# Optimization experiments

Measured on AMD Instinct MI355X. Metric: run time of the kernel, lower is better.

Reference implementation:

```python
import jax, jax.numpy as jnp
import numpy as np

B, N, FA, FP, C = 64, 64, 75, 14, 128


def _mlp2(x, W0, b0, W1, b1):
    # two lazy-Linear + ReLU sub-layers (n_sub_layer=2)
    h = jax.nn.relu(x @ W0 + b0)
    return jax.nn.relu(h @ W1 + b1)


def setup_inputs() -> dict:
    key = jax.random.key(0)
    ks = jax.random.split(key, 32)
    w = lambda k, s: jax.random.normal(k, s, jnp.float32) * 0.05
    inp = {
        "atom_x": jax.random.normal(ks[0], (B, N, FA), jnp.float32),
        "pair_x": jax.random.normal(ks[1], (B, N * N, FP), jnp.float32),
        # atom_to_atom: FA -> C -> C
        "a2a_W0": w(ks[2], (FA, C)), "a2a_b0": w(ks[3], (C,)),
        "a2a_W1": w(ks[4], (C, C)), "a2a_b1": w(ks[5], (C,)),
        # pair_to_atom: FP -> C -> C
        "p2a_W0": w(ks[6], (FP, C)), "p2a_b0": w(ks[7], (C,)),
        "p2a_W1": w(ks[8], (C, C)), "p2a_b1": w(ks[9], (C,)),
        # atom_layer: 2C -> C -> C
        "al_W0": w(ks[10], (2 * C, C)), "al_b0": w(ks[11], (C,)),
        "al_W1": w(ks[12], (C, C)), "al_b1": w(ks[13], (C,)),
        # atom_to_pair (weights shared across both orderings): 2FA -> C -> C
        "a2p_W0": w(ks[14], (2 * FA, C)), "a2p_b0": w(ks[15], (C,)),
        "a2p_W1": w(ks[16], (C, C)), "a2p_b1": w(ks[17], (C,)),
        # pair_to_pair: FP -> C -> C
        "p2p_W0": w(ks[18], (FP, C)), "p2p_b0": w(ks[19], (C,)),
        "p2p_W1": w(ks[20], (C, C)), "p2p_b1": w(ks[21], (C,)),
        # pair_layer: 2C -> C -> C
        "pl_W0": w(ks[22], (2 * C, C)), "pl_b0": w(ks[23], (C,)),
        "pl_W1": w(ks[24], (C, C)), "pl_b1": w(ks[25], (C,)),
    }
    return inp


def reference(atom_x, pair_x,
              a2a_W0, a2a_b0, a2a_W1, a2a_b1,
              p2a_W0, p2a_b0, p2a_W1, p2a_b1,
              al_W0, al_b0, al_W1, al_b1,
              a2p_W0, a2p_b0, a2p_W1, a2p_b1,
              p2p_W0, p2p_b0, p2p_W1, p2p_b1,
              pl_W0, pl_b0, pl_W1, pl_b1):
    b, n, fa = atom_x.shape
    # --- atom branch ---
    a0 = _mlp2(atom_x, a2a_W0, a2a_b0, a2a_W1, a2a_b1)            # [B,N,C]
    a1 = _mlp2(pair_x, p2a_W0, p2a_b0, p2a_W1, p2a_b1)            # [B,N*N,C]
    a1 = a1.reshape(b, n, n, -1).sum(axis=2)                      # PairToAtom sum
    a = jnp.concatenate([a0, a1], axis=-1)                        # [B,N,2C]
    next_atom = jax.nn.relu(_mlp2(a, al_W0, al_b0, al_W1, al_b1))  # extra relu per forward
    # --- pair branch ---
    rep = jnp.broadcast_to(atom_x[:, None, :, :], (b, n, n, fa))  # atom_repeat
    til = jnp.broadcast_to(atom_x[:, :, None, :], (b, n, n, fa))  # atom_tile
    pr0 = jnp.concatenate([til, rep], axis=-1).reshape(b, n * n, 2 * fa)
    pr1 = jnp.concatenate([rep, til], axis=-1).reshape(b, n * n, 2 * fa)
    p0 = (_mlp2(pr0, a2p_W0, a2p_b0, a2p_W1, a2p_b1)
          + _mlp2(pr1, a2p_W0, a2p_b0, a2p_W1, a2p_b1))            # [B,N*N,C]
    p1 = _mlp2(pair_x, p2p_W0, p2p_b0, p2p_W1, p2p_b1)            # [B,N*N,C]
    p = jnp.concatenate([p0, p1], axis=-1)                        # [B,N*N,2C]
    next_pair = jax.nn.relu(_mlp2(p, pl_W0, pl_b0, pl_W1, pl_b1))
    return (next_atom, next_pair)
```

## Files before the change

### kernel.cpp

```cpp
#include <hip/hip_runtime.h>
#include <hip/hip_bf16.h>

typedef unsigned short u16;
typedef unsigned int u32;
typedef __attribute__((ext_vector_type(8))) __bf16 bf16x8;
typedef __attribute__((ext_vector_type(4))) float f32x4;

#define B_ 64
#define N_ 64
#define FA_ 75
#define FP_ 14
#define C_ 128

__device__ float g_A0[4096 * 128];
__device__ float g_A1[4096 * 128];
__device__ float g_TB[4096 * 256];
__device__ u16   g_Wf[208896];

#define OFF_AA0   0
#define OFF_AA1   12288
#define OFF_APT   28672
#define OFF_APB   40960
#define OFF_PA0   53248
#define OFF_PA1   57344
#define OFF_AL0   73728
#define OFF_AL1   106496
#define OFF_AP1   122880
#define OFF_PP0   139264
#define OFF_PP1   143360
#define OFF_PL0T  159744
#define OFF_PL0B  176128
#define OFF_PL1   192512

__device__ __forceinline__ float bf2f(u16 a) {
    union { u32 u; float f; } v; v.u = ((u32)a) << 16; return v.f;
}
__device__ __forceinline__ u16 f2bf(float f) {
    union { float f; u32 u; } v; v.f = f;
    u32 r = v.u + 0x7fffu + ((v.u >> 16) & 1u);
    return (u16)(r >> 16);
}
#if __has_builtin(__builtin_amdgcn_cvt_pk_bf16_f32)
__device__ __forceinline__ u32 f2bf_pk(float a, float b) {
    auto r = __builtin_amdgcn_cvt_pk_bf16_f32(a, b);
    if constexpr (sizeof(r) == 4) {
        union { decltype(r) v; u32 u; } c; c.v = r; return c.u;
    } else {
        return (u32)f2bf(a) | ((u32)f2bf(b) << 16);
    }
}
#else
__device__ __forceinline__ u32 f2bf_pk(float a, float b) {
    return (u32)f2bf(a) | ((u32)f2bf(b) << 16);
}
#endif

__device__ __forceinline__ bool detect_isbf(const void* __restrict__ atom) {
    u32 wrd = ((const u32*)atom)[threadIdx.x & 63];
    u32 ex = (wrd >> 7) & 0xffu;
    unsigned long long m = __ballot(ex >= 113u && ex <= 133u);
    return __popcll(m) >= 32;
}

__device__ __forceinline__ float ldf(const void* p, size_t i, bool isbf) {
    if (isbf) return bf2f(((const u16*)p)[i]);
    return ((const float*)p)[i];
}
__device__ __forceinline__ f32x4 ldf4(const void* p, int i, bool isbf) {
    f32x4 r;
    if (isbf) {
        const u16* q = (const u16*)p + i;
        r[0] = bf2f(q[0]); r[1] = bf2f(q[1]); r[2] = bf2f(q[2]); r[3] = bf2f(q[3]);
    } else {
        r = *(const f32x4*)((const float*)p + i);
    }
    return r;
}
__device__ __forceinline__ uint4 pack8(const void* p, size_t base, int kmax, int k0, bool isbf) {
    uint4 u;
    if (isbf) {
        const u16* q = (const u16*)p + base;
        u16 h[8];
#pragma unroll
        for (int j = 0; j < 8; ++j) h[j] = (k0 + j < kmax) ? q[k0 + j] : (u16)0;
        u.x = (u32)h[0] | ((u32)h[1] << 16); u.y = (u32)h[2] | ((u32)h[3] << 16);
        u.z = (u32)h[4] | ((u32)h[5] << 16); u.w = (u32)h[6] | ((u32)h[7] << 16);
    } else {
        const float* q = (const float*)p + base;
        float f[8];
#pragma unroll
        for (int j = 0; j < 8; ++j) f[j] = (k0 + j < kmax) ? q[k0 + j] : 0.f;
        u.x = f2bf_pk(f[0], f[1]); u.y = f2bf_pk(f[2], f[3]);
        u.z = f2bf_pk(f[4], f[5]); u.w = f2bf_pk(f[6], f[7]);
    }
    return u;
}

__global__ __launch_bounds__(256) void prep_w(
    const void* atom,
    const void* aaW0, const void* aaW1, const void* apW0,
    const void* paW0, const void* paW1, const void* alW0, const void* alW1,
    const void* apW1, const void* ppW0, const void* ppW1,
    const void* plW0, const void* plW1) {
    const bool isbf = detect_isbf(atom);
    const void* srcs[14] = {aaW0, aaW1, apW0, apW0, paW0, paW1, alW0, alW1,
                            apW1, ppW0, ppW1, plW0, plW0, plW1};
    const int Ktab[14]  = {75, 128, 75, 75, 14, 128, 256, 128, 128, 14, 128, 128, 128, 128};
    const int KStab[14] = {3, 4, 3, 3, 1, 4, 8, 4, 4, 1, 4, 4, 4, 4};
    const int rofft[14] = {0, 0, 0, 75, 0, 0, 0, 0, 0, 0, 0, 0, 128, 0};
    const int baset[14] = {OFF_AA0, OFF_AA1, OFF_APT, OFF_APB, OFF_PA0, OFF_PA1,
                           OFF_AL0, OFF_AL1, OFF_AP1, OFF_PP0, OFF_PP1,
                           OFF_PL0T, OFF_PL0B, OFF_PL1};
    int gid = blockIdx.x * 256 + threadIdx.x;
    int j = 0, s = gid;
    while (j < 14 && s >= KStab[j] * 512) { s -= KStab[j] * 512; ++j; }
    if (j >= 14) return;
    int lane = s & 63, rest = s >> 6;
    int ks = rest % KStab[j], mt = rest / KStab[j];
    int m = mt * 16 + (lane & 15), q = lane >> 4;
    float f[8];
#pragma unroll
    for (int jj = 0; jj < 8; ++jj) {
        int k = ks * 32 + q * 8 + jj;
        f[jj] = (k < Ktab[j]) ? ldf(srcs[j], (size_t)(rofft[j] + k) * 128 + m, isbf) : 0.f;
    }
    uint4 u;
    u.x = f2bf_pk(f[0], f[1]); u.y = f2bf_pk(f[2], f[3]);
    u.z = f2bf_pk(f[4], f[5]); u.w = f2bf_pk(f[6], f[7]);
    *(uint4*)&g_Wf[(size_t)baset[j] + (size_t)s * 8] = u;
}

__device__ __forceinline__ bf16x8 as_bf(uint4 u) {
    union { uint4 u; bf16x8 b; } cv; cv.u = u; return cv.b;
}
template<int KS, int NT>
__device__ __forceinline__ void gemm2(const u16* __restrict__ wf,
                                      const u16* __restrict__ bF,
                                      int mt0, int lane, f32x4 (&acc)[2][NT]) {
#pragma unroll
    for (int ks = 0; ks < KS; ++ks) {
        bf16x8 a0 = *(const bf16x8*)(wf + (((mt0    ) * KS + ks) * 64 + lane) * 8);
        bf16x8 a1 = *(const bf16x8*)(wf + (((mt0 + 1) * KS + ks) * 64 + lane) * 8);
#pragma unroll
        for (int nt = 0; nt < NT; ++nt) {
            bf16x8 b = *(const bf16x8*)(bF + ((nt * KS + ks) * 64 + lane) * 8);
            acc[0][nt] = __builtin_amdgcn_mfma_f32_16x16x32_bf16(a0, b, acc[0][nt], 0, 0, 0);
            acc[1][nt] = __builtin_amdgcn_mfma_f32_16x16x32_bf16(a1, b, acc[1][nt], 0, 0, 0);
        }
    }
}
template<int KS>
__device__ __forceinline__ void loadA2(const u16* __restrict__ wf, int mt0, int lane,
                                       uint4 (&aw)[2][KS]) {
#pragma unroll
    for (int ks = 0; ks < KS; ++ks) {
        aw[0][ks] = *(const uint4*)(wf + (((mt0    ) * KS + ks) * 64 + lane) * 8);
        aw[1][ks] = *(const uint4*)(wf + (((mt0 + 1) * KS + ks) * 64 + lane) * 8);
    }
}
template<int KS, int NT>
__device__ __forceinline__ void gemm2r(const uint4 (&aw)[2][KS],
                                       const u16* __restrict__ bF,
                                       int lane, f32x4 (&acc)[2][NT]) {
#pragma unroll
    for (int ks = 0; ks < KS; ++ks) {
        bf16x8 a0 = as_bf(aw[0][ks]);
        bf16x8 a1 = as_bf(aw[1][ks]);
#pragma unroll
        for (int nt = 0; nt < NT; ++nt) {
            bf16x8 b = *(const bf16x8*)(bF + ((nt * KS + ks) * 64 + lane) * 8);
            acc[0][nt] = __builtin_amdgcn_mfma_f32_16x16x32_bf16(a0, b, acc[0][nt], 0, 0, 0);
            acc[1][nt] = __builtin_amdgcn_mfma_f32_16x16x32_bf16(a1, b, acc[1][nt], 0, 0, 0);
        }
    }
}

__device__ __forceinline__ void barrier_lgkm() {
    asm volatile("s_waitcnt lgkmcnt(0)" ::: "memory");
    __builtin_amdgcn_s_barrier();
    asm volatile("" ::: "memory");
}

__device__ __forceinline__ void frag_store(u16* dstF, int KSd, int nt, int mt, int lane, f32x4 v) {
    int c = lane & 15, quad = lane >> 4;
    int lp = c + 16 * ((2 * mt + (quad >> 1)) & 3);
    int ks = mt >> 1;
    uint2 u; u.x = f2bf_pk(v[0], v[1]); u.y = f2bf_pk(v[2], v[3]);
    *(uint2*)(dstF + (((nt * KSd + ks) * 64 + lp) * 8 + (quad & 1) * 4)) = u;
}

__device__ __forceinline__ void store_out4(void* outp, size_t elem, f32x4 v, bool isbf) {
    if (isbf) {
        uint2 u; u.x = f2bf_pk(v[0], v[1]); u.y = f2bf_pk(v[2], v[3]);
        *(uint2*)((u16*)outp + elem) = u;
    } else {
        *(f32x4*)((float*)outp + elem) = v;
    }
}

#define EPI_RELU_STORE(ACC, BB0, BB1, DST, NTN) do {                             \
    _Pragma("unroll") for (int ii = 0; ii < 2; ++ii) {                           \
        f32x4 bb_ = ii ? (BB1) : (BB0);                                          \
        _Pragma("unroll") for (int nt_ = 0; nt_ < NTN; ++nt_) {                  \
            f32x4 v_;                                                            \
            _Pragma("unroll") for (int r_ = 0; r_ < 4; ++r_) {                   \
                float x_ = ACC[ii][nt_][r_] + bb_[r_];                           \
                v_[r_] = x_ > 0.f ? x_ : 0.f;                                    \
            }                                                                    \
            frag_store(DST, 4, nt_, mt0 + ii, lane, v_);                         \
        }                                                                        \
    }                                                                            \
} while (0)

__global__ __launch_bounds__(256) void atom_pre(
    const void* __restrict__ atom,
    const void* __restrict__ aaB0, const void* __restrict__ aaB1) {
    __shared__ __align__(16) u16 sXF[2 * 3 * 64 * 8];
    __shared__ __align__(16) u16 sHF[2 * 4 * 64 * 8];
    const bool isbf = detect_isbf(atom);
    const int t = threadIdx.x, lane = t & 63, w = t >> 6;
    const int quad = lane >> 4;
    const int r0g = blockIdx.x * 32;
    for (int s = t; s < 2 * 3 * 64; s += 256) {
        int lane_s = s & 63, rest = s >> 6;
        int ks = rest % 3, nt = rest / 3;
        int n = nt * 16 + (lane_s & 15), q = lane_s >> 4;
        *(uint4*)&sXF[s * 8] = pack8(atom, (size_t)(r0g + n) * FA_, FA_, ks * 32 + q * 8, isbf);
    }
    __syncthreads();
    const int mt0 = 2 * w;
    {
        f32x4 bb0 = ldf4(aaB0, mt0 * 16 + quad * 4, isbf);
        f32x4 bb1 = ldf4(aaB0, (mt0 + 1) * 16 + quad * 4, isbf);
        f32x4 acc[2][2];
#pragma unroll
        for (int ii = 0; ii < 2; ++ii)
#pragma unroll
            for (int nt = 0; nt < 2; ++nt) acc[ii][nt] = (f32x4){0.f, 0.f, 0.f, 0.f};
        gemm2<3, 2>(g_Wf + OFF_AA0, sXF, mt0, lane, acc);
        EPI_RELU_STORE(acc, bb0, bb1, sHF, 2);
    }
    __syncthreads();
    {
        f32x4 bb0 = ldf4(aaB1, mt0 * 16 + quad * 4, isbf);
        f32x4 bb1 = ldf4(aaB1, (mt0 + 1) * 16 + quad * 4, isbf);
        f32x4 acc[2][2];
#pragma unroll
        for (int ii = 0; ii < 2; ++ii)
#pragma unroll
            for (int nt = 0; nt < 2; ++nt) acc[ii][nt] = (f32x4){0.f, 0.f, 0.f, 0.f};
        gemm2<4, 2>(g_Wf + OFF_AA1, sHF, mt0, lane, acc);
        int c = lane & 15;
#pragma unroll
        for (int ii = 0; ii < 2; ++ii) {
            int mt = mt0 + ii;
            f32x4 bb = ii ? bb1 : bb0;
#pragma unroll
            for (int nt = 0; nt < 2; ++nt) {
                f32x4 v;
#pragma unroll
                for (int r = 0; r < 4; ++r) { float x = acc[ii][nt][r] + bb[r]; v[r] = x > 0.f ? x : 0.f; }
                *(f32x4*)&g_A0[(size_t)(r0g + nt * 16 + c) * 128 + mt * 16 + quad * 4] = v;
            }
        }
    }
    {
        f32x4 accT[2][2], accB[2][2];
#pragma unroll
        for (int ii = 0; ii < 2; ++ii)
#pragma unroll
            for (int nt = 0; nt < 2; ++nt) { accT[ii][nt] = (f32x4){0.f,0.f,0.f,0.f}; accB[ii][nt] = (f32x4){0.f,0.f,0.f,0.f}; }
        gemm2<3, 2>(g_Wf + OFF_APT, sXF, mt0, lane, accT);
        gemm2<3, 2>(g_Wf + OFF_APB, sXF, mt0, lane, accB);
        int c = lane & 15;
#pragma unroll
        for (int ii = 0; ii < 2; ++ii) {
            int mt = mt0 + ii;
#pragma unroll
            for (int nt = 0; nt < 2; ++nt) {
                size_t row = (size_t)(r0g + nt * 16 + c);
                *(f32x4*)&g_TB[row * 256 + mt * 16 + quad * 4] = accT[ii][nt];
                *(f32x4*)&g_TB[row * 256 + 128 + mt * 16 + quad * 4] = accB[ii][nt];
            }
        }
    }
}

__global__ __launch_bounds__(256) void atom_layer(
    const void* __restrict__ atom,
    const void* __restrict__ alB0, const void* __restrict__ alB1,
    void* __restrict__ out) {
    __shared__ __align__(16) u16 sXF[1 * 8 * 64 * 8];
    __shared__ __align__(16) u16 sHF[1 * 4 * 64 * 8];
    const bool isbf = detect_isbf(atom);
    const int t = threadIdx.x, lane = t & 63, w = t >> 6;
    const int quad = lane >> 4;
    const int r0g = blockIdx.x * 16;
    for (int s = t; s < 8 * 64; s += 256) {
        int lane_s = s & 63, ks = s >> 6;
        int n = lane_s & 15, q = lane_s >> 4;
        int k0 = ks * 32 + q * 8;
        const float* src = (k0 < 128) ? &g_A0[(size_t)(r0g + n) * 128 + k0]
                                      : &g_A1[(size_t)(r0g + n) * 128 + (k0 - 128)];
        f32x4 f0 = *(const f32x4*)src, f1 = *(const f32x4*)(src + 4);
        uint4 u;
        u.x = f2bf_pk(f0[0], f0[1]); u.y = f2bf_pk(f0[2], f0[3]);
        u.z = f2bf_pk(f1[0], f1[1]); u.w = f2bf_pk(f1[2], f1[3]);
        *(uint4*)&sXF[s * 8] = u;
    }
    __syncthreads();
    const int mt0 = 2 * w;
    {
        f32x4 bb0 = ldf4(alB0, mt0 * 16 + quad * 4, isbf);
        f32x4 bb1 = ldf4(alB0, (mt0 + 1) * 16 + quad * 4, isbf);
        f32x4 acc[2][1];
#pragma unroll
        for (int ii = 0; ii < 2; ++ii) acc[ii][0] = (f32x4){0.f, 0.f, 0.f, 0.f};
        gemm2<8, 1>(g_Wf + OFF_AL0, sXF, mt0, lane, acc);
        EPI_RELU_STORE(acc, bb0, bb1, sHF, 1);
    }
    __syncthreads();
    {
        f32x4 bb0 = ldf4(alB1, mt0 * 16 + quad * 4, isbf);
        f32x4 bb1 = ldf4(alB1, (mt0 + 1) * 16 + quad * 4, isbf);
        f32x4 acc[2][1];
#pragma unroll
        for (int ii = 0; ii < 2; ++ii) acc[ii][0] = (f32x4){0.f, 0.f, 0.f, 0.f};
        gemm2<4, 1>(g_Wf + OFF_AL1, sHF, mt0, lane, acc);
        int c = lane & 15;
#pragma unroll
        for (int ii = 0; ii < 2; ++ii) {
            int mt = mt0 + ii;
            f32x4 bb = ii ? bb1 : bb0;
            f32x4 v;
#pragma unroll
            for (int r = 0; r < 4; ++r) { float x = acc[ii][0][r] + bb[r]; v[r] = x > 0.f ? x : 0.f; }
            store_out4(out, (size_t)(r0g + c) * 128 + mt * 16 + quad * 4, v, isbf);
        }
    }
}

__global__ __launch_bounds__(256, 3) void pair_fused(
    const void* __restrict__ atom,
    const void* __restrict__ pairx,
    const void* __restrict__ apB0, const void* __restrict__ apB1,
    const void* __restrict__ ppB0, const void* __restrict__ ppB1,
    const void* __restrict__ plB0, const void* __restrict__ plB1,
    const void* __restrict__ paB0, const void* __restrict__ paB1,
    void* __restrict__ out) {
    __shared__ __align__(16) u16 sX1[4 * 4 * 64 * 8];
    __shared__ __align__(16) u16 sX2[4 * 4 * 64 * 8];
    __shared__ __align__(16) u16 sR [4 * 4 * 64 * 8];
    __shared__ __align__(16) u16 sPr[4 * 1 * 64 * 8];
    const bool isbf = detect_isbf(atom);
    const int t = threadIdx.x, lane = t & 63, w = t >> 6;
    const int quad = lane >> 4, c = lane & 15;
    const int bx = blockIdx.x;
    const int b = bx >> 6, i = bx & 63;
    const int trow = b * 64;
    const size_t prow0 = (size_t)b * 4096 + (size_t)i * 64;
    const int mt0 = 2 * w;

    {
        int lane_s = t & 63, nt = t >> 6;
        int n = nt * 16 + (lane_s & 15), q = lane_s >> 4;
        *(uint4*)&sPr[t * 8] = pack8(pairx, (prow0 + n) * FP_, FP_, q * 8, isbf);
    }
    {
        const int ksg = t >> 6;
        const int k0 = ksg * 32 + quad * 8;
        const int rc = c;
        const float* TBi = &g_TB[(size_t)(trow + i) * 256 + k0];
        f32x4 t0 = *(const f32x4*)TBi,        t1 = *(const f32x4*)(TBi + 4);
        f32x4 o0 = *(const f32x4*)(TBi + 128), o1 = *(const f32x4*)(TBi + 132);
        f32x4 b0a = ldf4(apB0, k0, isbf), b0b = ldf4(apB0, k0 + 4, isbf);
        float Tip[8], Bip[8];
#pragma unroll
        for (int r = 0; r < 4; ++r) {
            Tip[r] = t0[r] + b0a[r]; Tip[4 + r] = t1[r] + b0b[r];
            Bip[r] = o0[r] + b0a[r]; Bip[4 + r] = o1[r] + b0b[r];
        }
#pragma unroll
        for (int nt = 0; nt < 4; ++nt) {
            int n = nt * 16 + rc;
            const float* Bj = &g_TB[(size_t)(trow + n) * 256 + k0];
            f32x4 j0 = *(const f32x4*)Bj,        j1 = *(const f32x4*)(Bj + 4);
            f32x4 j2 = *(const f32x4*)(Bj + 128), j3 = *(const f32x4*)(Bj + 132);
            float v0[8], v1[8];
#pragma unroll
            for (int r = 0; r < 4; ++r) {
                float x0 = Tip[r] + j2[r];      v0[r]     = x0 > 0.f ? x0 : 0.f;
                float x1 = Tip[4 + r] + j3[r];  v0[4 + r] = x1 > 0.f ? x1 : 0.f;
                float y0 = j0[r] + Bip[r];      v1[r]     = y0 > 0.f ? y0 : 0.f;
                float y1 = j1[r] + Bip[4 + r];  v1[4 + r] = y1 > 0.f ? y1 : 0.f;
            }
            uint4 u0, u1;
            u0.x = f2bf_pk(v0[0], v0[1]); u0.y = f2bf_pk(v0[2], v0[3]);
            u0.z = f2bf_pk(v0[4], v0[5]); u0.w = f2bf_pk(v0[6], v0[7]);
            u1.x = f2bf_pk(v1[0], v1[1]); u1.y = f2bf_pk(v1[2], v1[3]);
            u1.z = f2bf_pk(v1[4], v1[5]); u1.w = f2bf_pk(v1[6], v1[7]);
            int slot = ((nt * 4 + ksg) * 64 + lane) * 8;
            *(uint4*)&sX1[slot] = u0;
            *(uint4*)&sX2[slot] = u1;
        }
    }
    uint4 aAP1[2][4]; loadA2<4>(g_Wf + OFF_AP1, mt0, lane, aAP1);
    barrier_lgkm();
    {
        f32x4 bb0 = ldf4(apB1, mt0 * 16 + quad * 4, isbf);
        f32x4 bb1 = ldf4(apB1, (mt0 + 1) * 16 + quad * 4, isbf);
        f32x4 aA[2][4], aB[2][4];
#pragma unroll
        for (int ii = 0; ii < 2; ++ii)
#pragma unroll
            for (int nt = 0; nt < 4; ++nt) { aA[ii][nt] = (f32x4){0.f,0.f,0.f,0.f}; aB[ii][nt] = (f32x4){0.f,0.f,0.f,0.f}; }
        gemm2r<4, 4>(aAP1, sX1, lane, aA);
        gemm2r<4, 4>(aAP1, sX2, lane, aB);
#pragma unroll
        for (int ii = 0; ii < 2; ++ii) {
            int mt = mt0 + ii;
            f32x4 bb = ii ? bb1 : bb0;
#pragma unroll
            for (int nt = 0; nt < 4; ++nt) {
                f32x4 v;
#pragma unroll
                for (int r = 0; r < 4; ++r) {
                    float x = aA[ii][nt][r] + bb[r];
                    float y = aB[ii][nt][r] + bb[r];
                    v[r] = (x > 0.f ? x : 0.f) + (y > 0.f ? y : 0.f);
                }
                frag_store(sR, 4, nt, mt, lane, v);
            }
        }
    }
    f32x4 aH[2][4], aPA[2][4];
    {
        uint4 aPP0[2][1]; loadA2<1>(g_Wf + OFF_PP0, mt0, lane, aPP0);
        uint4 aPA0[2][1]; loadA2<1>(g_Wf + OFF_PA0, mt0, lane, aPA0);
#pragma unroll
        for (int ii = 0; ii < 2; ++ii)
#pragma unroll
            for (int nt = 0; nt < 4; ++nt) { aH[ii][nt] = (f32x4){0.f,0.f,0.f,0.f}; aPA[ii][nt] = (f32x4){0.f,0.f,0.f,0.f}; }
        gemm2r<1, 4>(aPP0, sPr, lane, aH);
        gemm2r<1, 4>(aPA0, sPr, lane, aPA);
    }
    uint4 aPL0T[2][4]; loadA2<4>(g_Wf + OFF_PL0T, mt0, lane, aPL0T);
    barrier_lgkm();
    f32x4 C3[2][4];
#pragma unroll
    for (int ii = 0; ii < 2; ++ii)
#pragma unroll
        for (int nt = 0; nt < 4; ++nt) C3[ii][nt] = (f32x4){0.f, 0.f, 0.f, 0.f};
    gemm2r<4, 4>(aPL0T, sR, lane, C3);
    {
        f32x4 bb0 = ldf4(ppB0, mt0 * 16 + quad * 4, isbf);
        f32x4 bb1 = ldf4(ppB0, (mt0 + 1) * 16 + quad * 4, isbf);
        EPI_RELU_STORE(aH, bb0, bb1, sX1, 4);
    }
    {
        f32x4 bb0 = ldf4(paB0, mt0 * 16 + quad * 4, isbf);
        f32x4 bb1 = ldf4(paB0, (mt0 + 1) * 16 + quad * 4, isbf);
        EPI_RELU_STORE(aPA, bb0, bb1, sX2, 4);
    }
    uint4 aPP1[2][4]; loadA2<4>(g_Wf + OFF_PP1, mt0, lane, aPP1);
    uint4 aPA1[2][4]; loadA2<4>(g_Wf + OFF_PA1, mt0, lane, aPA1);
    barrier_lgkm();
    {
        f32x4 aP[2][4], aA1[2][4];
#pragma unroll
        for (int ii = 0; ii < 2; ++ii)
#pragma unroll
            for (int nt = 0; nt < 4; ++nt) { aP[ii][nt] = (f32x4){0.f,0.f,0.f,0.f}; aA1[ii][nt] = (f32x4){0.f,0.f,0.f,0.f}; }
        gemm2r<4, 4>(aPP1, sX1, lane, aP);
        gemm2r<4, 4>(aPA1, sX2, lane, aA1);
        {
            f32x4 pb0 = ldf4(paB1, mt0 * 16 + quad * 4, isbf);
            f32x4 pb1 = ldf4(paB1, (mt0 + 1) * 16 + quad * 4, isbf);
#pragma unroll
            for (int ii = 0; ii < 2; ++ii) {
                int mt = mt0 + ii;
                f32x4 bb = ii ? pb1 : pb0;
                f32x4 ssum = (f32x4){0.f, 0.f, 0.f, 0.f};
#pragma unroll
                for (int nt = 0; nt < 4; ++nt)
#pragma unroll
                    for (int r = 0; r < 4; ++r) {
                        float x = aA1[ii][nt][r] + bb[r];
                        ssum[r] += (x > 0.f ? x : 0.f);
                    }
#pragma unroll
                for (int m = 1; m < 16; m <<= 1)
#pragma unroll
                    for (int r = 0; r < 4; ++r) ssum[r] += __shfl_xor(ssum[r], m, 64);
                if ((lane & 15) == 0)
                    *(f32x4*)&g_A1[(size_t)bx * 128 + mt * 16 + quad * 4] = ssum;
            }
        }
        f32x4 bb0 = ldf4(ppB1, mt0 * 16 + quad * 4, isbf);
        f32x4 bb1 = ldf4(ppB1, (mt0 + 1) * 16 + quad * 4, isbf);
        EPI_RELU_STORE(aP, bb0, bb1, sR, 4);
    }
    uint4 aPL0B[2][4]; loadA2<4>(g_Wf + OFF_PL0B, mt0, lane, aPL0B);
    barrier_lgkm();
    gemm2r<4, 4>(aPL0B, sR, lane, C3);
    {
        f32x4 bb0 = ldf4(plB0, mt0 * 16 + quad * 4, isbf);
        f32x4 bb1 = ldf4(plB0, (mt0 + 1) * 16 + quad * 4, isbf);
        EPI_RELU_STORE(C3, bb0, bb1, sX1, 4);
    }
    uint4 aPL1[2][4]; loadA2<4>(g_Wf + OFF_PL1, mt0, lane, aPL1);
    barrier_lgkm();
    {
        f32x4 bb0 = ldf4(plB1, mt0 * 16 + quad * 4, isbf);
        f32x4 bb1 = ldf4(plB1, (mt0 + 1) * 16 + quad * 4, isbf);
        f32x4 aO[2][4];
#pragma unroll
        for (int ii = 0; ii < 2; ++ii)
#pragma unroll
            for (int nt = 0; nt < 4; ++nt) aO[ii][nt] = (f32x4){0.f, 0.f, 0.f, 0.f};
        gemm2r<4, 4>(aPL1, sX1, lane, aO);
        const size_t NA = (size_t)B_ * N_ * C_;
#pragma unroll
        for (int ii = 0; ii < 2; ++ii) {
            int mt = mt0 + ii;
            f32x4 bb = ii ? bb1 : bb0;
#pragma unroll
            for (int nt = 0; nt < 4; ++nt) {
                f32x4 v;
#pragma unroll
                for (int r = 0; r < 4; ++r) { float x = aO[ii][nt][r] + bb[r]; v[r] = x > 0.f ? x : 0.f; }
                store_out4(out, NA + (prow0 + nt * 16 + c) * 128 + mt * 16 + quad * 4, v, isbf);
            }
        }
    }
}

extern "C" void kernel_launch(void* const* d_in, const int* in_sizes, int n_in,
                              void* d_out, int out_size, void* d_ws, size_t ws_size,
                              hipStream_t stream) {
    const void* atom  = d_in[0];
    const void* pairx = d_in[1];
    const void* aaW0 = d_in[2];  const void* aaB0 = d_in[3];
    const void* aaW1 = d_in[4];  const void* aaB1 = d_in[5];
    const void* paW0 = d_in[6];  const void* paB0 = d_in[7];
    const void* paW1 = d_in[8];  const void* paB1 = d_in[9];
    const void* alW0 = d_in[10]; const void* alB0 = d_in[11];
    const void* alW1 = d_in[12]; const void* alB1 = d_in[13];
    const void* apW0 = d_in[14]; const void* apB0 = d_in[15];
    const void* apW1 = d_in[16]; const void* apB1 = d_in[17];
    const void* ppW0 = d_in[18]; const void* ppB0 = d_in[19];
    const void* ppW1 = d_in[20]; const void* ppB1 = d_in[21];
    const void* plW0 = d_in[22]; const void* plB0 = d_in[23];
    const void* plW1 = d_in[24]; const void* plB1 = d_in[25];
    (void)d_ws; (void)ws_size; (void)in_sizes; (void)n_in; (void)out_size;

    prep_w<<<102, 256, 0, stream>>>(atom, aaW0, aaW1, apW0, paW0, paW1, alW0, alW1,
                                    apW1, ppW0, ppW1, plW0, plW1);
    atom_pre<<<128, 256, 0, stream>>>(atom, aaB0, aaB1);
    pair_fused<<<4096, 256, 0, stream>>>(atom, pairx, apB0, apB1, ppB0, ppB1,
                                         plB0, plB1, paB0, paB1, d_out);
    atom_layer<<<256, 256, 0, stream>>>(atom, alB0, alB1, d_out);
}
```

Before: 288.9 us.

## Fuse weight prep into atom pre-pass and raise wave priority around MFMA loops

Merges the weight-conversion kernel and the atom pre-pass into one launch. The first 76 blocks convert the weights the later kernels need, and the remaining blocks compute the atom branch, reading the FA-side weights directly from the raw inputs and converting them on the fly. This removes one kernel launch and its serialization point, at the cost of redundant per-block weight loads and conversion in the atom pre-pass. It also adds s_setprio around the MFMA GEMM calls in pair_fused to favour waves that are in their matrix phases.

```diff
diff --git a/kernel.cpp b/kernel.cpp
--- a/kernel.cpp
+++ b/kernel.cpp
@@ -17,10 +17,6 @@
 __device__ float g_TB[4096 * 256];
 __device__ u16   g_Wf[208896];
 
-#define OFF_AA0   0
-#define OFF_AA1   12288
-#define OFF_APT   28672
-#define OFF_APB   40960
 #define OFF_PA0   53248
 #define OFF_PA1   57344
 #define OFF_AL0   73728
@@ -95,39 +91,18 @@
     }
     return u;
 }
-
-__global__ __launch_bounds__(256) void prep_w(
-    const void* atom,
-    const void* aaW0, const void* aaW1, const void* apW0,
-    const void* paW0, const void* paW1, const void* alW0, const void* alW1,
-    const void* apW1, const void* ppW0, const void* ppW1,
-    const void* plW0, const void* plW1) {
-    const bool isbf = detect_isbf(atom);
-    const void* srcs[14] = {aaW0, aaW1, apW0, apW0, paW0, paW1, alW0, alW1,
-                            apW1, ppW0, ppW1, plW0, plW0, plW1};
-    const int Ktab[14]  = {75, 128, 75, 75, 14, 128, 256, 128, 128, 14, 128, 128, 128, 128};
-    const int KStab[14] = {3, 4, 3, 3, 1, 4, 8, 4, 4, 1, 4, 4, 4, 4};
-    const int rofft[14] = {0, 0, 0, 75, 0, 0, 0, 0, 0, 0, 0, 0, 128, 0};
-    const int baset[14] = {OFF_AA0, OFF_AA1, OFF_APT, OFF_APB, OFF_PA0, OFF_PA1,
-                           OFF_AL0, OFF_AL1, OFF_AP1, OFF_PP0, OFF_PP1,
-                           OFF_PL0T, OFF_PL0B, OFF_PL1};
-    int gid = blockIdx.x * 256 + threadIdx.x;
-    int j = 0, s = gid;
-    while (j < 14 && s >= KStab[j] * 512) { s -= KStab[j] * 512; ++j; }
-    if (j >= 14) return;
-    int lane = s & 63, rest = s >> 6;
-    int ks = rest % KStab[j], mt = rest / KStab[j];
-    int m = mt * 16 + (lane & 15), q = lane >> 4;
+__device__ __forceinline__ uint4 packW8(const void* W, int kmax, int rofft,
+                                        int k0, int m, bool isbf) {
     float f[8];
 #pragma unroll
-    for (int jj = 0; jj < 8; ++jj) {
-        int k = ks * 32 + q * 8 + jj;
-        f[jj] = (k < Ktab[j]) ? ldf(srcs[j], (size_t)(rofft[j] + k) * 128 + m, isbf) : 0.f;
+    for (int j = 0; j < 8; ++j) {
+        int k = k0 + j;
+        f[j] = (k < kmax) ? ldf(W, (size_t)(rofft + k) * 128 + m, isbf) : 0.f;
     }
     uint4 u;
     u.x = f2bf_pk(f[0], f[1]); u.y = f2bf_pk(f[2], f[3]);
     u.z = f2bf_pk(f[4], f[5]); u.w = f2bf_pk(f[6], f[7]);
-    *(uint4*)&g_Wf[(size_t)baset[j] + (size_t)s * 8] = u;
+    return u;
 }
 
 __device__ __forceinline__ bf16x8 as_bf(uint4 u) {
@@ -141,6 +116,24 @@
     for (int ks = 0; ks < KS; ++ks) {
         bf16x8 a0 = *(const bf16x8*)(wf + (((mt0    ) * KS + ks) * 64 + lane) * 8);
         bf16x8 a1 = *(const bf16x8*)(wf + (((mt0 + 1) * KS + ks) * 64 + lane) * 8);
+#pragma unroll
+        for (int nt = 0; nt < NT; ++nt) {
+            bf16x8 b = *(const bf16x8*)(bF + ((nt * KS + ks) * 64 + lane) * 8);
+            acc[0][nt] = __builtin_amdgcn_mfma_f32_16x16x32_bf16(a0, b, acc[0][nt], 0, 0, 0);
+            acc[1][nt] = __builtin_amdgcn_mfma_f32_16x16x32_bf16(a1, b, acc[1][nt], 0, 0, 0);
+        }
+    }
+}
+template<int KS, int NT>
+__device__ __forceinline__ void gemm2w(const void* W, int kmax, int rofft, bool isbf,
+                                       const u16* __restrict__ bF,
+                                       int mt0, int lane, f32x4 (&acc)[2][NT]) {
+    const int c = lane & 15, q = lane >> 4;
+#pragma unroll
+    for (int ks = 0; ks < KS; ++ks) {
+        int k0 = ks * 32 + q * 8;
+        bf16x8 a0 = as_bf(packW8(W, kmax, rofft, k0, mt0 * 16 + c, isbf));
+        bf16x8 a1 = as_bf(packW8(W, kmax, rofft, k0, (mt0 + 1) * 16 + c, isbf));
 #pragma unroll
         for (int nt = 0; nt < NT; ++nt) {
             bf16x8 b = *(const bf16x8*)(bF + ((nt * KS + ks) * 64 + lane) * 8);
@@ -212,15 +205,46 @@
     }                                                                            \
 } while (0)
 
-__global__ __launch_bounds__(256) void atom_pre(
-    const void* __restrict__ atom,
-    const void* __restrict__ aaB0, const void* __restrict__ aaB1) {
+__global__ __launch_bounds__(256) void pre_fused(
+    const void* atom,
+    const void* aaW0, const void* aaW1, const void* apW0,
+    const void* paW0, const void* paW1, const void* alW0, const void* alW1,
+    const void* apW1, const void* ppW0, const void* ppW1,
+    const void* plW0, const void* plW1,
+    const void* aaB0, const void* aaB1) {
     __shared__ __align__(16) u16 sXF[2 * 3 * 64 * 8];
     __shared__ __align__(16) u16 sHF[2 * 4 * 64 * 8];
     const bool isbf = detect_isbf(atom);
     const int t = threadIdx.x, lane = t & 63, w = t >> 6;
     const int quad = lane >> 4;
-    const int r0g = blockIdx.x * 32;
+    if (blockIdx.x < 76) {
+        const void* srcs[10] = {paW0, paW1, alW0, alW1, apW1, ppW0, ppW1,
+                                plW0, plW0, plW1};
+        const int Ktab[10]  = {14, 128, 256, 128, 128, 14, 128, 128, 128, 128};
+        const int KStab[10] = {1, 4, 8, 4, 4, 1, 4, 4, 4, 4};
+        const int rofft[10] = {0, 0, 0, 0, 0, 0, 0, 0, 128, 0};
+        const int baset[10] = {OFF_PA0, OFF_PA1, OFF_AL0, OFF_AL1, OFF_AP1,
+                               OFF_PP0, OFF_PP1, OFF_PL0T, OFF_PL0B, OFF_PL1};
+        int gid = blockIdx.x * 256 + t;
+        int j = 0, s = gid;
+        while (j < 10 && s >= KStab[j] * 512) { s -= KStab[j] * 512; ++j; }
+        if (j >= 10) return;
+        int ln = s & 63, rest = s >> 6;
+        int ks = rest % KStab[j], mt = rest / KStab[j];
+        int m = mt * 16 + (ln & 15), q = ln >> 4;
+        float f[8];
+#pragma unroll
+        for (int jj = 0; jj < 8; ++jj) {
+            int k = ks * 32 + q * 8 + jj;
+            f[jj] = (k < Ktab[j]) ? ldf(srcs[j], (size_t)(rofft[j] + k) * 128 + m, isbf) : 0.f;
+        }
+        uint4 u;
+        u.x = f2bf_pk(f[0], f[1]); u.y = f2bf_pk(f[2], f[3]);
+        u.z = f2bf_pk(f[4], f[5]); u.w = f2bf_pk(f[6], f[7]);
+        *(uint4*)&g_Wf[(size_t)baset[j] + (size_t)s * 8] = u;
+        return;
+    }
+    const int r0g = (blockIdx.x - 76) * 32;
     for (int s = t; s < 2 * 3 * 64; s += 256) {
         int lane_s = s & 63, rest = s >> 6;
         int ks = rest % 3, nt = rest / 3;
@@ -237,7 +261,7 @@
         for (int ii = 0; ii < 2; ++ii)
 #pragma unroll
             for (int nt = 0; nt < 2; ++nt) acc[ii][nt] = (f32x4){0.f, 0.f, 0.f, 0.f};
-        gemm2<3, 2>(g_Wf + OFF_AA0, sXF, mt0, lane, acc);
+        gemm2w<3, 2>(aaW0, 75, 0, isbf, sXF, mt0, lane, acc);
         EPI_RELU_STORE(acc, bb0, bb1, sHF, 2);
     }
     __syncthreads();
@@ -249,7 +273,7 @@
         for (int ii = 0; ii < 2; ++ii)
 #pragma unroll
             for (int nt = 0; nt < 2; ++nt) acc[ii][nt] = (f32x4){0.f, 0.f, 0.f, 0.f};
-        gemm2<4, 2>(g_Wf + OFF_AA1, sHF, mt0, lane, acc);
+        gemm2w<4, 2>(aaW1, 128, 0, isbf, sHF, mt0, lane, acc);
         int c = lane & 15;
 #pragma unroll
         for (int ii = 0; ii < 2; ++ii) {
@@ -270,8 +294,8 @@
         for (int ii = 0; ii < 2; ++ii)
 #pragma unroll
             for (int nt = 0; nt < 2; ++nt) { accT[ii][nt] = (f32x4){0.f,0.f,0.f,0.f}; accB[ii][nt] = (f32x4){0.f,0.f,0.f,0.f}; }
-        gemm2<3, 2>(g_Wf + OFF_APT, sXF, mt0, lane, accT);
-        gemm2<3, 2>(g_Wf + OFF_APB, sXF, mt0, lane, accB);
+        gemm2w<3, 2>(apW0, 75, 0, isbf, sXF, mt0, lane, accT);
+        gemm2w<3, 2>(apW0, 75, 75, isbf, sXF, mt0, lane, accB);
         int c = lane & 15;
 #pragma unroll
         for (int ii = 0; ii < 2; ++ii) {
@@ -414,8 +438,10 @@
         for (int ii = 0; ii < 2; ++ii)
 #pragma unroll
             for (int nt = 0; nt < 4; ++nt) { aA[ii][nt] = (f32x4){0.f,0.f,0.f,0.f}; aB[ii][nt] = (f32x4){0.f,0.f,0.f,0.f}; }
+        __builtin_amdgcn_s_setprio(1);
         gemm2r<4, 4>(aAP1, sX1, lane, aA);
         gemm2r<4, 4>(aAP1, sX2, lane, aB);
+        __builtin_amdgcn_s_setprio(0);
 #pragma unroll
         for (int ii = 0; ii < 2; ++ii) {
             int mt = mt0 + ii;
@@ -451,7 +477,9 @@
     for (int ii = 0; ii < 2; ++ii)
 #pragma unroll
         for (int nt = 0; nt < 4; ++nt) C3[ii][nt] = (f32x4){0.f, 0.f, 0.f, 0.f};
+    __builtin_amdgcn_s_setprio(1);
     gemm2r<4, 4>(aPL0T, sR, lane, C3);
+    __builtin_amdgcn_s_setprio(0);
     {
         f32x4 bb0 = ldf4(ppB0, mt0 * 16 + quad * 4, isbf);
         f32x4 bb1 = ldf4(ppB0, (mt0 + 1) * 16 + quad * 4, isbf);
@@ -471,8 +499,10 @@
         for (int ii = 0; ii < 2; ++ii)
 #pragma unroll
             for (int nt = 0; nt < 4; ++nt) { aP[ii][nt] = (f32x4){0.f,0.f,0.f,0.f}; aA1[ii][nt] = (f32x4){0.f,0.f,0.f,0.f}; }
+        __builtin_amdgcn_s_setprio(1);
         gemm2r<4, 4>(aPP1, sX1, lane, aP);
         gemm2r<4, 4>(aPA1, sX2, lane, aA1);
+        __builtin_amdgcn_s_setprio(0);
         {
             f32x4 pb0 = ldf4(paB1, mt0 * 16 + quad * 4, isbf);
             f32x4 pb1 = ldf4(paB1, (mt0 + 1) * 16 + quad * 4, isbf);
@@ -502,7 +532,9 @@
     }
     uint4 aPL0B[2][4]; loadA2<4>(g_Wf + OFF_PL0B, mt0, lane, aPL0B);
     barrier_lgkm();
+    __builtin_amdgcn_s_setprio(1);
     gemm2r<4, 4>(aPL0B, sR, lane, C3);
+    __builtin_amdgcn_s_setprio(0);
     {
         f32x4 bb0 = ldf4(plB0, mt0 * 16 + quad * 4, isbf);
         f32x4 bb1 = ldf4(plB0, (mt0 + 1) * 16 + quad * 4, isbf);
@@ -518,7 +550,9 @@
         for (int ii = 0; ii < 2; ++ii)
 #pragma unroll
             for (int nt = 0; nt < 4; ++nt) aO[ii][nt] = (f32x4){0.f, 0.f, 0.f, 0.f};
+        __builtin_amdgcn_s_setprio(1);
         gemm2r<4, 4>(aPL1, sX1, lane, aO);
+        __builtin_amdgcn_s_setprio(0);
         const size_t NA = (size_t)B_ * N_ * C_;
 #pragma unroll
         for (int ii = 0; ii < 2; ++ii) {
@@ -554,9 +588,9 @@
     const void* plW1 = d_in[24]; const void* plB1 = d_in[25];
     (void)d_ws; (void)ws_size; (void)in_sizes; (void)n_in; (void)out_size;
 
-    prep_w<<<102, 256, 0, stream>>>(atom, aaW0, aaW1, apW0, paW0, paW1, alW0, alW1,
-                                    apW1, ppW0, ppW1, plW0, plW1);
-    atom_pre<<<128, 256, 0, stream>>>(atom, aaB0, aaB1);
+    pre_fused<<<204, 256, 0, stream>>>(atom, aaW0, aaW1, apW0, paW0, paW1,
+                                       alW0, alW1, apW1, ppW0, ppW1, plW0, plW1,
+                                       aaB0, aaB1);
     pair_fused<<<4096, 256, 0, stream>>>(atom, pairx, apB0, apB1, ppB0, ppB1,
                                          plB0, plB1, paB0, paB1, d_out);
     atom_layer<<<256, 256, 0, stream>>>(atom, alB0, alB1, d_out);
```

New measurement: 294.1 us. About the same (+1.8%).

## Split atom kernels into smaller blocks, preload weights to registers, raise MFMA wave priority

Applied to the files above, without the earlier changes.

atom_pre now handles 16 rows per block and atom_layer 8 rows per block, which doubles the grid sizes to spread the small atom kernels over more CUs. Both kernels preload their weight fragments into registers before the LDS barrier so the global loads overlap with staging, and they use the register-operand GEMM. Each MFMA GEMM section in pair_fused is wrapped in s_setprio(1)/s_setprio(0) to favour matrix issue. atom_layer pads 16-wide MFMA tiles over only 8 real rows, so half its compute is wasted and it needs a row clamp and a store mask.

```diff
diff --git a/kernel.cpp b/kernel.cpp
--- a/kernel.cpp
+++ b/kernel.cpp
@@ -215,73 +215,64 @@
 __global__ __launch_bounds__(256) void atom_pre(
     const void* __restrict__ atom,
     const void* __restrict__ aaB0, const void* __restrict__ aaB1) {
-    __shared__ __align__(16) u16 sXF[2 * 3 * 64 * 8];
-    __shared__ __align__(16) u16 sHF[2 * 4 * 64 * 8];
+    __shared__ __align__(16) u16 sXF[3 * 64 * 8];
+    __shared__ __align__(16) u16 sHF[4 * 64 * 8];
     const bool isbf = detect_isbf(atom);
     const int t = threadIdx.x, lane = t & 63, w = t >> 6;
     const int quad = lane >> 4;
-    const int r0g = blockIdx.x * 32;
-    for (int s = t; s < 2 * 3 * 64; s += 256) {
-        int lane_s = s & 63, rest = s >> 6;
-        int ks = rest % 3, nt = rest / 3;
-        int n = nt * 16 + (lane_s & 15), q = lane_s >> 4;
+    const int r0g = blockIdx.x * 16;
+    const int mt0 = 2 * w;
+    uint4 aAA0[2][3]; loadA2<3>(g_Wf + OFF_AA0, mt0, lane, aAA0);
+    for (int s = t; s < 3 * 64; s += 256) {
+        int lane_s = s & 63, ks = s >> 6;
+        int n = lane_s & 15, q = lane_s >> 4;
         *(uint4*)&sXF[s * 8] = pack8(atom, (size_t)(r0g + n) * FA_, FA_, ks * 32 + q * 8, isbf);
     }
-    __syncthreads();
-    const int mt0 = 2 * w;
+    uint4 aAA1[2][4]; loadA2<4>(g_Wf + OFF_AA1, mt0, lane, aAA1);
+    barrier_lgkm();
     {
         f32x4 bb0 = ldf4(aaB0, mt0 * 16 + quad * 4, isbf);
         f32x4 bb1 = ldf4(aaB0, (mt0 + 1) * 16 + quad * 4, isbf);
-        f32x4 acc[2][2];
-#pragma unroll
-        for (int ii = 0; ii < 2; ++ii)
-#pragma unroll
-            for (int nt = 0; nt < 2; ++nt) acc[ii][nt] = (f32x4){0.f, 0.f, 0.f, 0.f};
-        gemm2<3, 2>(g_Wf + OFF_AA0, sXF, mt0, lane, acc);
-        EPI_RELU_STORE(acc, bb0, bb1, sHF, 2);
-    }
-    __syncthreads();
+        f32x4 acc[2][1];
+#pragma unroll
+        for (int ii = 0; ii < 2; ++ii) acc[ii][0] = (f32x4){0.f, 0.f, 0.f, 0.f};
+        gemm2r<3, 1>(aAA0, sXF, lane, acc);
+        EPI_RELU_STORE(acc, bb0, bb1, sHF, 1);
+    }
+    uint4 aAPT[2][3]; loadA2<3>(g_Wf + OFF_APT, mt0, lane, aAPT);
+    uint4 aAPB[2][3]; loadA2<3>(g_Wf + OFF_APB, mt0, lane, aAPB);
+    barrier_lgkm();
     {
         f32x4 bb0 = ldf4(aaB1, mt0 * 16 + quad * 4, isbf);
         f32x4 bb1 = ldf4(aaB1, (mt0 + 1) * 16 + quad * 4, isbf);
-        f32x4 acc[2][2];
-#pragma unroll
-        for (int ii = 0; ii < 2; ++ii)
-#pragma unroll
-            for (int nt = 0; nt < 2; ++nt) acc[ii][nt] = (f32x4){0.f, 0.f, 0.f, 0.f};
-        gemm2<4, 2>(g_Wf + OFF_AA1, sHF, mt0, lane, acc);
+        f32x4 acc[2][1];
+#pragma unroll
+        for (int ii = 0; ii < 2; ++ii) acc[ii][0] = (f32x4){0.f, 0.f, 0.f, 0.f};
+        gemm2r<4, 1>(aAA1, sHF, lane, acc);
         int c = lane & 15;
 #pragma unroll
         for (int ii = 0; ii < 2; ++ii) {
             int mt = mt0 + ii;
             f32x4 bb = ii ? bb1 : bb0;
-#pragma unroll
-            for (int nt = 0; nt < 2; ++nt) {
-                f32x4 v;
-#pragma unroll
-                for (int r = 0; r < 4; ++r) { float x = acc[ii][nt][r] + bb[r]; v[r] = x > 0.f ? x : 0.f; }
-                *(f32x4*)&g_A0[(size_t)(r0g + nt * 16 + c) * 128 + mt * 16 + quad * 4] = v;
-            }
-        }
-    }
-    {
-        f32x4 accT[2][2], accB[2][2];
-#pragma unroll
-        for (int ii = 0; ii < 2; ++ii)
-#pragma unroll
-            for (int nt = 0; nt < 2; ++nt) { accT[ii][nt] = (f32x4){0.f,0.f,0.f,0.f}; accB[ii][nt] = (f32x4){0.f,0.f,0.f,0.f}; }
-        gemm2<3, 2>(g_Wf + OFF_APT, sXF, mt0, lane, accT);
-        gemm2<3, 2>(g_Wf + OFF_APB, sXF, mt0, lane, accB);
+            f32x4 v;
+#pragma unroll
+            for (int r = 0; r < 4; ++r) { float x = acc[ii][0][r] + bb[r]; v[r] = x > 0.f ? x : 0.f; }
+            *(f32x4*)&g_A0[(size_t)(r0g + c) * 128 + mt * 16 + quad * 4] = v;
+        }
+    }
+    {
+        f32x4 accT[2][1], accB[2][1];
+#pragma unroll
+        for (int ii = 0; ii < 2; ++ii) { accT[ii][0] = (f32x4){0.f,0.f,0.f,0.f}; accB[ii][0] = (f32x4){0.f,0.f,0.f,0.f}; }
+        gemm2r<3, 1>(aAPT, sXF, lane, accT);
+        gemm2r<3, 1>(aAPB, sXF, lane, accB);
         int c = lane & 15;
 #pragma unroll
         for (int ii = 0; ii < 2; ++ii) {
             int mt = mt0 + ii;
-#pragma unroll
-            for (int nt = 0; nt < 2; ++nt) {
-                size_t row = (size_t)(r0g + nt * 16 + c);
-                *(f32x4*)&g_TB[row * 256 + mt * 16 + quad * 4] = accT[ii][nt];
-                *(f32x4*)&g_TB[row * 256 + 128 + mt * 16 + quad * 4] = accB[ii][nt];
-            }
+            size_t row = (size_t)(r0g + c);
+            *(f32x4*)&g_TB[row * 256 + mt * 16 + quad * 4] = accT[ii][0];
+            *(f32x4*)&g_TB[row * 256 + 128 + mt * 16 + quad * 4] = accB[ii][0];
         }
     }
 }
@@ -290,52 +281,57 @@
     const void* __restrict__ atom,
     const void* __restrict__ alB0, const void* __restrict__ alB1,
     void* __restrict__ out) {
-    __shared__ __align__(16) u16 sXF[1 * 8 * 64 * 8];
-    __shared__ __align__(16) u16 sHF[1 * 4 * 64 * 8];
+    __shared__ __align__(16) u16 sXF[8 * 64 * 8];
+    __shared__ __align__(16) u16 sHF[4 * 64 * 8];
     const bool isbf = detect_isbf(atom);
     const int t = threadIdx.x, lane = t & 63, w = t >> 6;
     const int quad = lane >> 4;
-    const int r0g = blockIdx.x * 16;
+    const int r0g = blockIdx.x * 8;
+    const int mt0 = 2 * w;
+    uint4 aAL0[2][8]; loadA2<8>(g_Wf + OFF_AL0, mt0, lane, aAL0);
     for (int s = t; s < 8 * 64; s += 256) {
         int lane_s = s & 63, ks = s >> 6;
         int n = lane_s & 15, q = lane_s >> 4;
+        int row = r0g + n; if (row > 4095) row = 4095;
         int k0 = ks * 32 + q * 8;
-        const float* src = (k0 < 128) ? &g_A0[(size_t)(r0g + n) * 128 + k0]
-                                      : &g_A1[(size_t)(r0g + n) * 128 + (k0 - 128)];
+        const float* src = (k0 < 128) ? &g_A0[(size_t)row * 128 + k0]
+                                      : &g_A1[(size_t)row * 128 + (k0 - 128)];
         f32x4 f0 = *(const f32x4*)src, f1 = *(const f32x4*)(src + 4);
         uint4 u;
         u.x = f2bf_pk(f0[0], f0[1]); u.y = f2bf_pk(f0[2], f0[3]);
         u.z = f2bf_pk(f1[0], f1[1]); u.w = f2bf_pk(f1[2], f1[3]);
         *(uint4*)&sXF[s * 8] = u;
     }
-    __syncthreads();
-    const int mt0 = 2 * w;
+    uint4 aAL1[2][4]; loadA2<4>(g_Wf + OFF_AL1, mt0, lane, aAL1);
+    barrier_lgkm();
     {
         f32x4 bb0 = ldf4(alB0, mt0 * 16 + quad * 4, isbf);
         f32x4 bb1 = ldf4(alB0, (mt0 + 1) * 16 + quad * 4, isbf);
         f32x4 acc[2][1];
 #pragma unroll
         for (int ii = 0; ii < 2; ++ii) acc[ii][0] = (f32x4){0.f, 0.f, 0.f, 0.f};
-        gemm2<8, 1>(g_Wf + OFF_AL0, sXF, mt0, lane, acc);
+        gemm2r<8, 1>(aAL0, sXF, lane, acc);
         EPI_RELU_STORE(acc, bb0, bb1, sHF, 1);
     }
-    __syncthreads();
+    barrier_lgkm();
     {
         f32x4 bb0 = ldf4(alB1, mt0 * 16 + quad * 4, isbf);
         f32x4 bb1 = ldf4(alB1, (mt0 + 1) * 16 + quad * 4, isbf);
         f32x4 acc[2][1];
 #pragma unroll
         for (int ii = 0; ii < 2; ++ii) acc[ii][0] = (f32x4){0.f, 0.f, 0.f, 0.f};
-        gemm2<4, 1>(g_Wf + OFF_AL1, sHF, mt0, lane, acc);
+        gemm2r<4, 1>(aAL1, sHF, lane, acc);
         int c = lane & 15;
-#pragma unroll
-        for (int ii = 0; ii < 2; ++ii) {
-            int mt = mt0 + ii;
-            f32x4 bb = ii ? bb1 : bb0;
-            f32x4 v;
-#pragma unroll
-            for (int r = 0; r < 4; ++r) { float x = acc[ii][0][r] + bb[r]; v[r] = x > 0.f ? x : 0.f; }
-            store_out4(out, (size_t)(r0g + c) * 128 + mt * 16 + quad * 4, v, isbf);
+        if (c < 8) {
+#pragma unroll
+            for (int ii = 0; ii < 2; ++ii) {
+                int mt = mt0 + ii;
+                f32x4 bb = ii ? bb1 : bb0;
+                f32x4 v;
+#pragma unroll
+                for (int r = 0; r < 4; ++r) { float x = acc[ii][0][r] + bb[r]; v[r] = x > 0.f ? x : 0.f; }
+                store_out4(out, (size_t)(r0g + c) * 128 + mt * 16 + quad * 4, v, isbf);
+            }
         }
     }
 }
@@ -414,8 +410,10 @@
         for (int ii = 0; ii < 2; ++ii)
 #pragma unroll
             for (int nt = 0; nt < 4; ++nt) { aA[ii][nt] = (f32x4){0.f,0.f,0.f,0.f}; aB[ii][nt] = (f32x4){0.f,0.f,0.f,0.f}; }
+        __builtin_amdgcn_s_setprio(1);
         gemm2r<4, 4>(aAP1, sX1, lane, aA);
         gemm2r<4, 4>(aAP1, sX2, lane, aB);
+        __builtin_amdgcn_s_setprio(0);
 #pragma unroll
         for (int ii = 0; ii < 2; ++ii) {
             int mt = mt0 + ii;
@@ -451,7 +449,9 @@
     for (int ii = 0; ii < 2; ++ii)
 #pragma unroll
         for (int nt = 0; nt < 4; ++nt) C3[ii][nt] = (f32x4){0.f, 0.f, 0.f, 0.f};
+    __builtin_amdgcn_s_setprio(1);
     gemm2r<4, 4>(aPL0T, sR, lane, C3);
+    __builtin_amdgcn_s_setprio(0);
     {
         f32x4 bb0 = ldf4(ppB0, mt0 * 16 + quad * 4, isbf);
         f32x4 bb1 = ldf4(ppB0, (mt0 + 1) * 16 + quad * 4, isbf);
@@ -471,8 +471,10 @@
         for (int ii = 0; ii < 2; ++ii)
 #pragma unroll
             for (int nt = 0; nt < 4; ++nt) { aP[ii][nt] = (f32x4){0.f,0.f,0.f,0.f}; aA1[ii][nt] = (f32x4){0.f,0.f,0.f,0.f}; }
+        __builtin_amdgcn_s_setprio(1);
         gemm2r<4, 4>(aPP1, sX1, lane, aP);
         gemm2r<4, 4>(aPA1, sX2, lane, aA1);
+        __builtin_amdgcn_s_setprio(0);
         {
             f32x4 pb0 = ldf4(paB1, mt0 * 16 + quad * 4, isbf);
             f32x4 pb1 = ldf4(paB1, (mt0 + 1) * 16 + quad * 4, isbf);
@@ -502,7 +504,9 @@
     }
     uint4 aPL0B[2][4]; loadA2<4>(g_Wf + OFF_PL0B, mt0, lane, aPL0B);
     barrier_lgkm();
+    __builtin_amdgcn_s_setprio(1);
     gemm2r<4, 4>(aPL0B, sR, lane, C3);
+    __builtin_amdgcn_s_setprio(0);
     {
         f32x4 bb0 = ldf4(plB0, mt0 * 16 + quad * 4, isbf);
         f32x4 bb1 = ldf4(plB0, (mt0 + 1) * 16 + quad * 4, isbf);
@@ -518,7 +522,9 @@
         for (int ii = 0; ii < 2; ++ii)
 #pragma unroll
             for (int nt = 0; nt < 4; ++nt) aO[ii][nt] = (f32x4){0.f, 0.f, 0.f, 0.f};
+        __builtin_amdgcn_s_setprio(1);
         gemm2r<4, 4>(aPL1, sX1, lane, aO);
+        __builtin_amdgcn_s_setprio(0);
         const size_t NA = (size_t)B_ * N_ * C_;
 #pragma unroll
         for (int ii = 0; ii < 2; ++ii) {
@@ -556,8 +562,8 @@
 
     prep_w<<<102, 256, 0, stream>>>(atom, aaW0, aaW1, apW0, paW0, paW1, alW0, alW1,
                                     apW1, ppW0, ppW1, plW0, plW1);
-    atom_pre<<<128, 256, 0, stream>>>(atom, aaB0, aaB1);
+    atom_pre<<<256, 256, 0, stream>>>(atom, aaB0, aaB1);
     pair_fused<<<4096, 256, 0, stream>>>(atom, pairx, apB0, apB1, ppB0, ppB1,
                                          plB0, plB1, paB0, paB1, d_out);
-    atom_layer<<<256, 256, 0, stream>>>(atom, alB0, alB1, d_out);
-}
+    atom_layer<<<512, 256, 0, stream>>>(atom, alB0, alB1, d_out);
+}
```

After: 288.9 us. Within noise of the previous version (+0.0%).
